# Kernel optimization log

Measured on AMD Instinct MI355X. Metric: run time of the kernel, lower is better.

## Reference

```python
import jax, jax.numpy as jnp
import numpy as np

KERNEL = 25  # hard-coded moving-average kernel in the torch Model
HID = 128


def moving_avg(x):
    # x: [B, L, C]; edge-pad (KERNEL-1)//2 on each side along time, then mean over window
    p = (KERNEL - 1) // 2
    front = jnp.repeat(x[:, 0:1, :], p, axis=1)
    end = jnp.repeat(x[:, -1:, :], p, axis=1)
    xp = jnp.concatenate([front, x, end], axis=1)  # [B, L+2p, C]
    cs = jnp.cumsum(xp, axis=1)
    cs = jnp.concatenate([jnp.zeros_like(cs[:, :1, :]), cs], axis=1)
    return (cs[:, KERNEL:, :] - cs[:, :-KERNEL, :]) / KERNEL  # [B, L, C]


def memory_enhance(repres, memory):
    # repres: [N, 128], memory: [F, 128]
    attention = jax.nn.softmax(jnp.einsum('nd,fd->nf', repres, memory), axis=1)
    output = jnp.einsum('nf,fd->nd', attention, memory)
    return jnp.concatenate([output, repres], axis=1)  # [N, 256]


def setup_inputs() -> dict:
    key = jax.random.key(0)
    ks = jax.random.split(key, 12)
    B, L, C, P, M = 128, 720, 321, 336, 512
    s = lambda k, shape, fan: jax.random.normal(k, shape, jnp.float32) * (1.0 / np.sqrt(fan))
    return {
        'x': jax.random.normal(ks[0], (B, L, C), jnp.float32),
        'W_s1': s(ks[1], (HID, L), L), 'b_s1': jnp.zeros((HID,), jnp.float32),
        'W_s2': s(ks[2], (P, 2 * HID), 2 * HID), 'b_s2': jnp.zeros((P,), jnp.float32),
        'W_t1': s(ks[3], (HID, L), L), 'b_t1': jnp.zeros((HID,), jnp.float32),
        'W_t2': s(ks[4], (P, 2 * HID), 2 * HID), 'b_t2': jnp.zeros((P,), jnp.float32),
        'mem_S': s(ks[5], (M, HID), HID),
        'mem_T': s(ks[6], (M, HID), HID),
    }


def reference(x, W_s1, b_s1, W_s2, b_s2, W_t1, b_t1, W_t2, b_t2, mem_S, mem_T):
    B, L, C = x.shape
    trend = moving_avg(x)                 # [B, L, C]
    seasonal = x - trend
    seasonal = jnp.transpose(seasonal, (0, 2, 1))  # [B, C, L]
    trend = jnp.transpose(trend, (0, 2, 1))

    def branch(init, W1, b1, mem, W2, b2):
        r = jax.nn.sigmoid(jnp.einsum('bcl,hl->bch', init, W1) + b1)  # [B, C, 128]
        r = r.reshape(-1, HID)
        r = memory_enhance(r, mem)                                    # [N, 256]
        r = r.reshape(B, C, 2 * HID)
        return jnp.einsum('bcd,pd->bcp', r, W2) + b2                  # [B, C, P]

    seasonal_out = branch(seasonal, W_s1, b_s1, mem_S, W_s2, b_s2)
    trend_out = branch(trend, W_t1, b_t1, mem_T, W_t2, b_t2)
    return jnp.transpose(seasonal_out + trend_out, (0, 2, 1))  # [B, P, C]
```

## Files before the change

kernel.cpp:

```cpp
#include <hip/hip_runtime.h>
#include <math.h>

#define BB 128
#define LL 720
#define CC 321
#define HH 128
#define PP 336
#define MM 512
#define LPAD 736

typedef __attribute__((ext_vector_type(8))) short bf16x8;
typedef __attribute__((ext_vector_type(4))) float f32x4;

__device__ __forceinline__ short f2bf(float x) {
  unsigned u = __builtin_bit_cast(unsigned, x);
  u = (u + 0x7FFFu + ((u >> 16) & 1u)) >> 16;
  return (short)u;
}

__device__ __forceinline__ bf16x8 ldfrag(const short* p) {
  short4 a = *(const short4*)p;
  short4 b = *(const short4*)(p + 16);
  bf16x8 r;
  r[0] = a.x; r[1] = a.y; r[2] = a.z; r[3] = a.w;
  r[4] = b.x; r[5] = b.y; r[6] = b.z; r[7] = b.w;
  return r;
}

__device__ __forceinline__ int4 stage_chunk(const short* g) {
  int2 lo = *(const int2*)g;
  int2 hi = *(const int2*)(g + 16);
  int4 r;
  r.x = lo.x; r.y = lo.y; r.z = hi.x; r.w = hi.y;
  return r;
}

__device__ __forceinline__ bf16x8 ldsfragP(const short* tile, int h, int lg) {
  return *(const bf16x8*)&tile[h * 40 + lg * 8];
}

__device__ __forceinline__ void gload_lds16(const short* g, short* l) {
  __builtin_amdgcn_global_load_lds(
      (const __attribute__((address_space(1))) unsigned int*)g,
      (__attribute__((address_space(3))) unsigned int*)l, 16, 0, 0);
}

__global__ void weff_kernel(const float* __restrict__ Ws1,
                            const float* __restrict__ Wt1,
                            short* __restrict__ WsT,
                            short* __restrict__ WtT) {
  int idx = blockIdx.x * 256 + threadIdx.x;
  if (idx >= HH * LPAD) return;
  int j = idx % LPAD, h = idx / LPAD;
  if (j >= LL) { WsT[idx] = 0; WtT[idx] = 0; return; }
  float ss = 0.f, st = 0.f;
  if (j == 0) {
    for (int l = 0; l <= 12; ++l) {
      float w = 13.f - (float)l;
      ss += w * Ws1[h * LL + l];
      st += w * Wt1[h * LL + l];
    }
  } else if (j == LL - 1) {
    for (int d = 0; d <= 12; ++d) {
      float w = 13.f - (float)d;
      ss += w * Ws1[h * LL + LL - 1 - d];
      st += w * Wt1[h * LL + LL - 1 - d];
    }
  } else {
    int lo = j - 12 < 0 ? 0 : j - 12;
    int hi = j + 12 > LL - 1 ? LL - 1 : j + 12;
    for (int l = lo; l <= hi; ++l) {
      ss += Ws1[h * LL + l];
      st += Wt1[h * LL + l];
    }
  }
  ss *= (1.f / 25.f);
  st *= (1.f / 25.f);
  WsT[idx] = f2bf(Ws1[h * LL + j] - ss);
  WtT[idx] = f2bf(st);
}

__global__ void memstage_kernel(const float* __restrict__ memS,
                                const float* __restrict__ memT,
                                short* __restrict__ stgS,
                                short* __restrict__ stgT) {
  int e = blockIdx.x * 256 + threadIdx.x;
  int br = e >> 14;
  int s = e & 16383;
  const float* src = br ? memT : memS;
  short* dst = br ? stgT : stgS;
  int tt = s >> 11;
  int c = s & 2047;
  int row = c >> 4, slot = c & 15;
  int sp = slot ^ (row & 7);
  int k = sp >> 2, lg = sp & 3;
  int ft = tt >> 1;
  short out[8];
  if ((tt & 1) == 0) {
    const float* r0 = src + (size_t)(ft * 128 + row) * 128 + k * 32 + lg * 4;
#pragma unroll
    for (int j = 0; j < 4; ++j) {
      out[j] = f2bf(r0[j]);
      out[j + 4] = f2bf(r0[16 + j]);
    }
  } else {
    int fbase = ft * 128 + k * 32 + lg * 4;
#pragma unroll
    for (int j = 0; j < 4; ++j) {
      out[j] = f2bf(src[(size_t)(fbase + j) * 128 + row]);
      out[j + 4] = f2bf(src[(size_t)(fbase + 16 + j) * 128 + row]);
    }
  }
  short4 a = make_short4(out[0], out[1], out[2], out[3]);
  short4 b = make_short4(out[4], out[5], out[6], out[7]);
  *(short4*)&dst[(size_t)s * 8] = a;
  *(short4*)&dst[(size_t)s * 8 + 4] = b;
}

__global__ void w2cvt_kernel(const float* __restrict__ Ws2,
                             const float* __restrict__ Wt2,
                             const float* __restrict__ bs2,
                             const float* __restrict__ bt2,
                             short* __restrict__ W2b, float* __restrict__ b2) {
  int i = blockIdx.x * 256 + threadIdx.x;
  if (i < PP) b2[i] = bs2[i] + bt2[i];
  if (i >= PP * 512) return;
  int p = i >> 9, k = i & 511;
  float v = (k < 256) ? Ws2[p * 256 + k] : Wt2[p * 256 + (k - 256)];
  W2b[i] = f2bf(v);
}

__global__ __launch_bounds__(256) void gemm1_mfma(
    const float* __restrict__ x,
    const short* __restrict__ WsT, const short* __restrict__ WtT,
    const float* __restrict__ bs1, const float* __restrict__ bt1,
    short* __restrict__ r2s, short* __restrict__ r2t) {
  __shared__ __align__(16) short wlds[2][2][128 * 40];
  int tid = threadIdx.x;
  int w = tid >> 6, l = tid & 63, lr = l & 15, lg = l >> 4;
  int n = blockIdx.x * 64 + w * 16 + lr;
  int b = n / CC;
  int c = n - b * CC;
  const float* xb = x + (size_t)b * (LL * CC) + c;

  int row0 = tid >> 2, q = tid & 3;
  const short* gS0 = WsT + row0 * LPAD + q * 4;
  const short* gS1 = gS0 + 64 * LPAD;
  const short* gT0 = WtT + row0 * LPAD + q * 4;
  const short* gT1 = gT0 + 64 * LPAD;
  int d0 = row0 * 40 + q * 8;
  int d1 = d0 + 64 * 40;

  f32x4 acc[2][8];
#pragma unroll
  for (int br = 0; br < 2; ++br)
#pragma unroll
    for (int i = 0; i < 8; ++i) acc[br][i] = (f32x4){0.f, 0.f, 0.f, 0.f};

  {
    int4 a = stage_chunk(gS0), bch = stage_chunk(gS1);
    int4 cch = stage_chunk(gT0), dch = stage_chunk(gT1);
    *(int4*)&wlds[0][0][d0] = a;
    *(int4*)&wlds[0][0][d1] = bch;
    *(int4*)&wlds[0][1][d0] = cch;
    *(int4*)&wlds[0][1][d1] = dch;
  }
  float xc[8];
#pragma unroll
  for (int j = 0; j < 4; ++j) {
    xc[j] = xb[(size_t)(lg * 4 + j) * CC];
    xc[j + 4] = xb[(size_t)(lg * 4 + j + 16) * CC];
  }
  __syncthreads();

  int cur = 0;
  for (int step = 0; step < 23; ++step) {
    bf16x8 bx;
#pragma unroll
    for (int j = 0; j < 8; ++j) bx[j] = f2bf(xc[j]);

    int4 nS0 = {0, 0, 0, 0}, nS1 = nS0, nT0 = nS0, nT1 = nS0;
    float xn[8] = {0.f};
    if (step < 22) {
      int ko = (step + 1) * 32;
      nS0 = stage_chunk(gS0 + ko);
      nS1 = stage_chunk(gS1 + ko);
      nT0 = stage_chunk(gT0 + ko);
      nT1 = stage_chunk(gT1 + ko);
#pragma unroll
      for (int j = 0; j < 4; ++j) {
        int k1 = ko + lg * 4 + j;
        int k2 = k1 + 16;
        xn[j] = xb[(size_t)k1 * CC];
        xn[j + 4] = (k2 < LL) ? xb[(size_t)k2 * CC] : 0.f;
      }
    }

    const short* tS = &wlds[cur][0][0];
    const short* tT = &wlds[cur][1][0];
#pragma unroll
    for (int ht = 0; ht < 8; ++ht) {
      bf16x8 aS = ldsfragP(tS, ht * 16 + lr, lg);
      bf16x8 aT = ldsfragP(tT, ht * 16 + lr, lg);
      acc[0][ht] =
          __builtin_amdgcn_mfma_f32_16x16x32_bf16(aS, bx, acc[0][ht], 0, 0, 0);
      acc[1][ht] =
          __builtin_amdgcn_mfma_f32_16x16x32_bf16(aT, bx, acc[1][ht], 0, 0, 0);
    }

    if (step < 22) {
      short* bS = &wlds[cur ^ 1][0][0];
      short* bT = &wlds[cur ^ 1][1][0];
      *(int4*)&bS[d0] = nS0;
      *(int4*)&bS[d1] = nS1;
      *(int4*)&bT[d0] = nT0;
      *(int4*)&bT[d1] = nT1;
    }
    __syncthreads();
#pragma unroll
    for (int j = 0; j < 8; ++j) xc[j] = xn[j];
    cur ^= 1;
  }

  short* rowS = r2s + (size_t)n * 256 + 128;
  short* rowT = r2t + (size_t)n * 256 + 128;
#pragma unroll
  for (int ht = 0; ht < 8; ++ht) {
    int h = ht * 16 + lg * 4;
    float4 bS = *(const float4*)&bs1[h];
    float4 bT = *(const float4*)&bt1[h];
    const float* pbS = &bS.x;
    const float* pbT = &bT.x;
    short4 ss, st;
    short* ps = &ss.x;
    short* pt = &st.x;
#pragma unroll
    for (int j = 0; j < 4; ++j) {
      ps[j] = f2bf(1.f / (1.f + __expf(-(acc[0][ht][j] + pbS[j]))));
      pt[j] = f2bf(1.f / (1.f + __expf(-(acc[1][ht][j] + pbT[j]))));
    }
    *(short4*)&rowS[h] = ss;
    *(short4*)&rowT[h] = st;
  }
}

__global__ __launch_bounds__(256) void memenh_mfma(
    const short* __restrict__ stgS, const short* __restrict__ stgT,
    short* __restrict__ r2s, short* __restrict__ r2t) {
  int br = blockIdx.y;
  const short* stg = br ? stgT : stgS;
  short* r2 = br ? r2t : r2s;

  __shared__ __align__(16) short buf[2][16384];
  int tid = threadIdx.x;
  int l = tid & 63, lr = l & 15, lg = l >> 4;
  int wbase = tid & 192;
  int n = blockIdx.x * 64 + (tid >> 6) * 16 + lr;

  bf16x8 brag[4];
  {
    const short* rb = r2 + (size_t)n * 256 + 128;
#pragma unroll
    for (int k = 0; k < 4; ++k) brag[k] = ldfrag(rb + k * 32 + lg * 4);
  }

#define STAGE(t, bsel)                                                        \
  {                                                                           \
    const short* g = stg + (size_t)(t)*16384;                                 \
    _Pragma("unroll") for (int i = 0; i < 8; ++i) {                           \
      gload_lds16(g + (size_t)(i * 256 + tid) * 8,                            \
                  &buf[bsel][(i * 256 + wbase) * 8]);                         \
    }                                                                         \
  }

  STAGE(0, 0);
  __syncthreads();

  f32x4 accO[8];
#pragma unroll
  for (int i = 0; i < 8; ++i) accO[i] = (f32x4){0.f, 0.f, 0.f, 0.f};
  bf16x8 pb[4];
  float ssum = 0.f;
  int cur = 0;

#pragma unroll
  for (int t = 0; t < 8; ++t) {
    if (t < 7) STAGE(t + 1, cur ^ 1);
    const short* tb = &buf[cur][0];
    if ((t & 1) == 0) {
      f32x4 sc[8];
#pragma unroll
      for (int ft16 = 0; ft16 < 8; ++ft16) {
        f32x4 a = {0.f, 0.f, 0.f, 0.f};
#pragma unroll
        for (int k = 0; k < 4; ++k) {
          int row = ft16 * 16 + lr;
          int slot = (4 * k + lg) ^ (row & 7);
          bf16x8 af = *(const bf16x8*)&tb[row * 128 + slot * 8];
          a = __builtin_amdgcn_mfma_f32_16x16x32_bf16(af, brag[k], a, 0, 0, 0);
        }
        sc[ft16] = a;
      }
#pragma unroll
      for (int i = 0; i < 8; ++i) {
        f32x4 v = sc[i];
#pragma unroll
        for (int j = 0; j < 4; ++j) {
          float e = __expf(v[j]);
          v[j] = e;
          ssum += e;
        }
        sc[i] = v;
      }
#pragma unroll
      for (int t4 = 0; t4 < 4; ++t4) {
        f32x4 e0 = sc[2 * t4], e1 = sc[2 * t4 + 1];
        bf16x8 f;
        f[0] = f2bf(e0[0]); f[1] = f2bf(e0[1]);
        f[2] = f2bf(e0[2]); f[3] = f2bf(e0[3]);
        f[4] = f2bf(e1[0]); f[5] = f2bf(e1[1]);
        f[6] = f2bf(e1[2]); f[7] = f2bf(e1[3]);
        pb[t4] = f;
      }
    } else {
#pragma unroll
      for (int dt = 0; dt < 8; ++dt) {
#pragma unroll
        for (int k = 0; k < 4; ++k) {
          int row = dt * 16 + lr;
          int slot = (4 * k + lg) ^ (row & 7);
          bf16x8 af = *(const bf16x8*)&tb[row * 128 + slot * 8];
          accO[dt] =
              __builtin_amdgcn_mfma_f32_16x16x32_bf16(af, pb[k], accO[dt], 0, 0, 0);
        }
      }
    }
    __syncthreads();
    cur ^= 1;
  }
#undef STAGE

  ssum += __shfl_xor(ssum, 16);
  ssum += __shfl_xor(ssum, 32);
  float inv = 1.f / ssum;
  short* rowO = r2 + (size_t)n * 256;
#pragma unroll
  for (int dt = 0; dt < 8; ++dt) {
    short4 o;
    o.x = f2bf(accO[dt][0] * inv);
    o.y = f2bf(accO[dt][1] * inv);
    o.z = f2bf(accO[dt][2] * inv);
    o.w = f2bf(accO[dt][3] * inv);
    *(short4*)&rowO[dt * 16 + lg * 4] = o;
  }
}

__global__ __launch_bounds__(512) void gemm2_mfma(
    const short* __restrict__ r2s, const short* __restrict__ r2t,
    const short* __restrict__ W2b,
    const float* __restrict__ b2,
    float* __restrict__ out) {
  __shared__ __align__(16) short w2lds[2][112 * 40];
  int tid = threadIdx.x;
  int w = tid >> 6, l = tid & 63, lr = l & 15, lg = l >> 4;
  int p0 = blockIdx.y * 112;
  int n = blockIdx.x * 128 + w * 16 + lr;
  int b = n / CC, c = n - b * CC;
  const short* rs = r2s + (size_t)n * 256;
  const short* rt = r2t + (size_t)n * 256;

  bool dostage = tid < 448;
  int row = tid >> 2, q = tid & 3;
  const short* gW = W2b + (size_t)(p0 + row) * 512 + q * 4;
  int doff = row * 40 + q * 8;

  f32x4 acc[7];
#pragma unroll
  for (int i = 0; i < 7; ++i) acc[i] = (f32x4){0.f, 0.f, 0.f, 0.f};

  if (dostage) *(int4*)&w2lds[0][doff] = stage_chunk(gW);
  __syncthreads();

  int cur = 0;
  for (int step = 0; step < 16; ++step) {
    int k0 = step * 32;
    const short* rrow = ((k0 < 256) ? rs : rt) + (k0 & 255);
    bf16x8 bfr = ldfrag(rrow + lg * 4);
    int4 nxt = {0, 0, 0, 0};
    if (step < 15 && dostage) nxt = stage_chunk(gW + (step + 1) * 32);
    const short* tw = &w2lds[cur][0];
#pragma unroll
    for (int pt = 0; pt < 7; ++pt) {
      bf16x8 a = ldsfragP(tw, pt * 16 + lr, lg);
      acc[pt] = __builtin_amdgcn_mfma_f32_16x16x32_bf16(a, bfr, acc[pt], 0, 0, 0);
    }
    if (step < 15 && dostage) *(int4*)&w2lds[cur ^ 1][doff] = nxt;
    __syncthreads();
    cur ^= 1;
  }

  size_t obase = (size_t)b * ((size_t)PP * CC) + c;
#pragma unroll
  for (int pt = 0; pt < 7; ++pt) {
    int p = p0 + pt * 16 + lg * 4;
    float4 bias = *(const float4*)&b2[p];
    const float* pb = &bias.x;
#pragma unroll
    for (int j = 0; j < 4; ++j) {
      out[obase + (size_t)(p + j) * CC] = acc[pt][j] + pb[j];
    }
  }
}

extern "C" void kernel_launch(void* const* d_in, const int* in_sizes, int n_in,
                              void* d_out, int out_size, void* d_ws, size_t ws_size,
                              hipStream_t stream) {
  const float* x    = (const float*)d_in[0];
  const float* Ws1  = (const float*)d_in[1];
  const float* bs1  = (const float*)d_in[2];
  const float* Ws2  = (const float*)d_in[3];
  const float* bs2  = (const float*)d_in[4];
  const float* Wt1  = (const float*)d_in[5];
  const float* bt1  = (const float*)d_in[6];
  const float* Wt2  = (const float*)d_in[7];
  const float* bt2  = (const float*)d_in[8];
  const float* memS = (const float*)d_in[9];
  const float* memT = (const float*)d_in[10];
  float* out = (float*)d_out;

  const size_t N = (size_t)BB * CC;
  short* r2s  = (short*)d_ws;
  short* r2t  = r2s + N * 256;
  short* WsTb = r2t + N * 256;
  short* WtTb = WsTb + (size_t)HH * LPAD;
  short* stgS = WtTb + (size_t)HH * LPAD;
  short* stgT = stgS + (size_t)16384 * 8;
  short* W2b  = stgT + (size_t)16384 * 8;
  float* b2   = (float*)(W2b + (size_t)PP * 512);

  weff_kernel<<<(HH * LPAD) / 256, 256, 0, stream>>>(Ws1, Wt1, WsTb, WtTb);
  memstage_kernel<<<128, 256, 0, stream>>>(memS, memT, stgS, stgT);
  w2cvt_kernel<<<(PP * 512) / 256, 256, 0, stream>>>(Ws2, Wt2, bs2, bt2, W2b, b2);

  gemm1_mfma<<<642, 256, 0, stream>>>(x, WsTb, WtTb, bs1, bt1, r2s, r2t);

  dim3 g3(642, 2);
  memenh_mfma<<<g3, 256, 0, stream>>>(stgS, stgT, r2s, r2t);

  dim3 g2(321, 3);
  gemm2_mfma<<<g2, 512, 0, stream>>>(r2s, r2t, W2b, b2, out);
}
```

Before: 152.0 us.

## Retile gemm1 warps to 32 rows by 64 hidden units for fragment reuse

Each wave in gemm1 now computes 32 sequence rows times half of the 128 hidden units, instead of 16 rows times all 128. Each weight fragment read from LDS therefore feeds two MFMAs, which halves the LDS fragment reads per MFMA. Weight staging becomes one contiguous 16-byte global load per chunk, and the permuted LDS layout is undone by a split read. Each wave now loads twice as many strided x values, which may raise uncoalesced global traffic and register pressure.

Result: slower. 166.2 us (+9.4%).

```diff
diff --git a/kernel.cpp b/kernel.cpp
--- a/kernel.cpp
+++ b/kernel.cpp
@@ -37,6 +37,15 @@
 
 __device__ __forceinline__ bf16x8 ldsfragP(const short* tile, int h, int lg) {
   return *(const bf16x8*)&tile[h * 40 + lg * 8];
+}
+
+__device__ __forceinline__ bf16x8 ldsfragR(const short* tile, int h, int lg) {
+  int2 lo = *(const int2*)&tile[h * 40 + lg * 4];
+  int2 hi = *(const int2*)&tile[h * 40 + lg * 4 + 16];
+  union { int2 v[2]; bf16x8 f; } u;
+  u.v[0] = lo;
+  u.v[1] = hi;
+  return u.f;
 }
 
 __device__ __forceinline__ void gload_lds16(const short* g, short* l) {
@@ -138,109 +147,139 @@
   __shared__ __align__(16) short wlds[2][2][128 * 40];
   int tid = threadIdx.x;
   int w = tid >> 6, l = tid & 63, lr = l & 15, lg = l >> 4;
-  int n = blockIdx.x * 64 + w * 16 + lr;
-  int b = n / CC;
-  int c = n - b * CC;
-  const float* xb = x + (size_t)b * (LL * CC) + c;
-
-  int row0 = tid >> 2, q = tid & 3;
-  const short* gS0 = WsT + row0 * LPAD + q * 4;
-  const short* gS1 = gS0 + 64 * LPAD;
-  const short* gT0 = WtT + row0 * LPAD + q * 4;
-  const short* gT1 = gT0 + 64 * LPAD;
-  int d0 = row0 * 40 + q * 8;
-  int d1 = d0 + 64 * 40;
-
-  f32x4 acc[2][8];
+  int ngrp = w >> 1, hhalf = w & 1;
+  int n0 = blockIdx.x * 64 + ngrp * 32 + lr;
+  int n1 = n0 + 16;
+  int b0 = n0 / CC, c0 = n0 - b0 * CC;
+  int b1 = n1 / CC, c1 = n1 - b1 * CC;
+  const float* xb0 = x + (size_t)b0 * (LL * CC) + c0;
+  const float* xb1 = x + (size_t)b1 * (LL * CC) + c1;
+
+  int rowA = tid >> 2, cqA = tid & 3;
+  int rowB = (tid + 256) >> 2, cqB = tid & 3;
+  const short* gSA = WsT + rowA * LPAD + cqA * 8;
+  const short* gSB = WsT + rowB * LPAD + cqB * 8;
+  const short* gTA = WtT + rowA * LPAD + cqA * 8;
+  const short* gTB = WtT + rowB * LPAD + cqB * 8;
+  int dA = rowA * 40 + cqA * 8;
+  int dB = rowB * 40 + cqB * 8;
+
+  f32x4 acc[2][4][2];
 #pragma unroll
   for (int br = 0; br < 2; ++br)
 #pragma unroll
-    for (int i = 0; i < 8; ++i) acc[br][i] = (f32x4){0.f, 0.f, 0.f, 0.f};
+    for (int i = 0; i < 4; ++i)
+#pragma unroll
+      for (int rt = 0; rt < 2; ++rt) acc[br][i][rt] = (f32x4){0.f, 0.f, 0.f, 0.f};
 
   {
-    int4 a = stage_chunk(gS0), bch = stage_chunk(gS1);
-    int4 cch = stage_chunk(gT0), dch = stage_chunk(gT1);
-    *(int4*)&wlds[0][0][d0] = a;
-    *(int4*)&wlds[0][0][d1] = bch;
-    *(int4*)&wlds[0][1][d0] = cch;
-    *(int4*)&wlds[0][1][d1] = dch;
-  }
-  float xc[8];
+    int4 sA = *(const int4*)gSA;
+    int4 sB = *(const int4*)gSB;
+    int4 tA = *(const int4*)gTA;
+    int4 tB = *(const int4*)gTB;
+    *(int4*)&wlds[0][0][dA] = sA;
+    *(int4*)&wlds[0][0][dB] = sB;
+    *(int4*)&wlds[0][1][dA] = tA;
+    *(int4*)&wlds[0][1][dB] = tB;
+  }
+  float xc0[8], xc1[8];
 #pragma unroll
   for (int j = 0; j < 4; ++j) {
-    xc[j] = xb[(size_t)(lg * 4 + j) * CC];
-    xc[j + 4] = xb[(size_t)(lg * 4 + j + 16) * CC];
+    int k1 = lg * 4 + j, k2 = k1 + 16;
+    xc0[j] = xb0[(size_t)k1 * CC];
+    xc0[j + 4] = xb0[(size_t)k2 * CC];
+    xc1[j] = xb1[(size_t)k1 * CC];
+    xc1[j + 4] = xb1[(size_t)k2 * CC];
   }
   __syncthreads();
 
+  int hb = hhalf * 64;
   int cur = 0;
   for (int step = 0; step < 23; ++step) {
-    bf16x8 bx;
-#pragma unroll
-    for (int j = 0; j < 8; ++j) bx[j] = f2bf(xc[j]);
-
-    int4 nS0 = {0, 0, 0, 0}, nS1 = nS0, nT0 = nS0, nT1 = nS0;
-    float xn[8] = {0.f};
+    int4 nSA = {0, 0, 0, 0}, nSB = nSA, nTA = nSA, nTB = nSA;
+    float xn0[8] = {0.f}, xn1[8] = {0.f};
     if (step < 22) {
       int ko = (step + 1) * 32;
-      nS0 = stage_chunk(gS0 + ko);
-      nS1 = stage_chunk(gS1 + ko);
-      nT0 = stage_chunk(gT0 + ko);
-      nT1 = stage_chunk(gT1 + ko);
+      nSA = *(const int4*)(gSA + ko);
+      nSB = *(const int4*)(gSB + ko);
+      nTA = *(const int4*)(gTA + ko);
+      nTB = *(const int4*)(gTB + ko);
 #pragma unroll
       for (int j = 0; j < 4; ++j) {
         int k1 = ko + lg * 4 + j;
         int k2 = k1 + 16;
-        xn[j] = xb[(size_t)k1 * CC];
-        xn[j + 4] = (k2 < LL) ? xb[(size_t)k2 * CC] : 0.f;
-      }
+        bool ok = k2 < LL;
+        xn0[j] = xb0[(size_t)k1 * CC];
+        xn0[j + 4] = ok ? xb0[(size_t)k2 * CC] : 0.f;
+        xn1[j] = xb1[(size_t)k1 * CC];
+        xn1[j + 4] = ok ? xb1[(size_t)k2 * CC] : 0.f;
+      }
+    }
+
+    bf16x8 bx0, bx1;
+#pragma unroll
+    for (int j = 0; j < 8; ++j) {
+      bx0[j] = f2bf(xc0[j]);
+      bx1[j] = f2bf(xc1[j]);
     }
 
     const short* tS = &wlds[cur][0][0];
     const short* tT = &wlds[cur][1][0];
 #pragma unroll
-    for (int ht = 0; ht < 8; ++ht) {
-      bf16x8 aS = ldsfragP(tS, ht * 16 + lr, lg);
-      bf16x8 aT = ldsfragP(tT, ht * 16 + lr, lg);
-      acc[0][ht] =
-          __builtin_amdgcn_mfma_f32_16x16x32_bf16(aS, bx, acc[0][ht], 0, 0, 0);
-      acc[1][ht] =
-          __builtin_amdgcn_mfma_f32_16x16x32_bf16(aT, bx, acc[1][ht], 0, 0, 0);
+    for (int ht = 0; ht < 4; ++ht) {
+      int h = hb + ht * 16 + lr;
+      bf16x8 aS = ldsfragR(tS, h, lg);
+      bf16x8 aT = ldsfragR(tT, h, lg);
+      acc[0][ht][0] =
+          __builtin_amdgcn_mfma_f32_16x16x32_bf16(aS, bx0, acc[0][ht][0], 0, 0, 0);
+      acc[0][ht][1] =
+          __builtin_amdgcn_mfma_f32_16x16x32_bf16(aS, bx1, acc[0][ht][1], 0, 0, 0);
+      acc[1][ht][0] =
+          __builtin_amdgcn_mfma_f32_16x16x32_bf16(aT, bx0, acc[1][ht][0], 0, 0, 0);
+      acc[1][ht][1] =
+          __builtin_amdgcn_mfma_f32_16x16x32_bf16(aT, bx1, acc[1][ht][1], 0, 0, 0);
     }
 
     if (step < 22) {
       short* bS = &wlds[cur ^ 1][0][0];
       short* bT = &wlds[cur ^ 1][1][0];
-      *(int4*)&bS[d0] = nS0;
-      *(int4*)&bS[d1] = nS1;
-      *(int4*)&bT[d0] = nT0;
-      *(int4*)&bT[d1] = nT1;
+      *(int4*)&bS[dA] = nSA;
+      *(int4*)&bS[dB] = nSB;
+      *(int4*)&bT[dA] = nTA;
+      *(int4*)&bT[dB] = nTB;
     }
     __syncthreads();
 #pragma unroll
-    for (int j = 0; j < 8; ++j) xc[j] = xn[j];
+    for (int j = 0; j < 8; ++j) {
+      xc0[j] = xn0[j];
+      xc1[j] = xn1[j];
+    }
     cur ^= 1;
   }
 
-  short* rowS = r2s + (size_t)n * 256 + 128;
-  short* rowT = r2t + (size_t)n * 256 + 128;
-#pragma unroll
-  for (int ht = 0; ht < 8; ++ht) {
-    int h = ht * 16 + lg * 4;
-    float4 bS = *(const float4*)&bs1[h];
-    float4 bT = *(const float4*)&bt1[h];
-    const float* pbS = &bS.x;
-    const float* pbT = &bT.x;
-    short4 ss, st;
-    short* ps = &ss.x;
-    short* pt = &st.x;
-#pragma unroll
-    for (int j = 0; j < 4; ++j) {
-      ps[j] = f2bf(1.f / (1.f + __expf(-(acc[0][ht][j] + pbS[j]))));
-      pt[j] = f2bf(1.f / (1.f + __expf(-(acc[1][ht][j] + pbT[j]))));
-    }
-    *(short4*)&rowS[h] = ss;
-    *(short4*)&rowT[h] = st;
+#pragma unroll
+  for (int rt = 0; rt < 2; ++rt) {
+    int n = rt ? n1 : n0;
+    short* rowS = r2s + (size_t)n * 256 + 128;
+    short* rowT = r2t + (size_t)n * 256 + 128;
+#pragma unroll
+    for (int ht = 0; ht < 4; ++ht) {
+      int h = hb + ht * 16 + lg * 4;
+      float4 bS = *(const float4*)&bs1[h];
+      float4 bT = *(const float4*)&bt1[h];
+      const float* pbS = &bS.x;
+      const float* pbT = &bT.x;
+      short4 ss, st;
+      short* ps = &ss.x;
+      short* pt = &st.x;
+#pragma unroll
+      for (int j = 0; j < 4; ++j) {
+        ps[j] = f2bf(1.f / (1.f + __expf(-(acc[0][ht][rt][j] + pbS[j]))));
+        pt[j] = f2bf(1.f / (1.f + __expf(-(acc[1][ht][rt][j] + pbT[j]))));
+      }
+      *(short4*)&rowS[h] = ss;
+      *(short4*)&rowT[h] = st;
+    }
   }
 }
 
```
